# Kernel tuning notes

Measured on AMD Instinct MI355X. Metric: run time of the kernel, lower is better.

## Reference

```python
import jax, jax.numpy as jnp
import numpy as np

B, S, A, C = 32, 52, 3, 80  # batch, grid, anchors-per-cell, classes
EPS_LOG = 1e-16
EPS_IOU = 1e-6
L_CLASS, L_NOOBJ, L_OBJ, L_BOX = 1.0, 10.0, 1.0, 10.0


def setup_inputs() -> dict:
    key = jax.random.key(0)
    k_obj, k_xy, k_wh, k_cls, k_pred, k_anc = jax.random.split(key, 6)
    # target (B,S,S,3,6): [obj_flag, x, y, w, h, class_id]
    obj = (jax.random.uniform(k_obj, (B, S, S, A)) < 0.05).astype(jnp.float32)
    xy = jax.random.uniform(k_xy, (B, S, S, A, 2))
    wh = jax.random.uniform(k_wh, (B, S, S, A, 2), minval=0.1, maxval=2.0)
    cls = jax.random.randint(k_cls, (B, S, S, A), 0, C).astype(jnp.float32)
    target = jnp.concatenate([obj[..., None], xy, wh, cls[..., None]], axis=-1)
    pred = jax.random.normal(k_pred, (B, S, S, A * (C + 5)), dtype=jnp.float32)
    anchors = jax.random.uniform(k_anc, (A, 2), minval=0.5, maxval=2.0)
    return {"target": target, "pred": pred, "anchors": anchors}


def _iou_midpoint(b1, b2):
    # boxes [..., 4] = (cx, cy, w, h)
    b1x1, b1y1 = b1[..., 0] - b1[..., 2] / 2, b1[..., 1] - b1[..., 3] / 2
    b1x2, b1y2 = b1[..., 0] + b1[..., 2] / 2, b1[..., 1] + b1[..., 3] / 2
    b2x1, b2y1 = b2[..., 0] - b2[..., 2] / 2, b2[..., 1] - b2[..., 3] / 2
    b2x2, b2y2 = b2[..., 0] + b2[..., 2] / 2, b2[..., 1] + b2[..., 3] / 2
    iw = jnp.clip(jnp.minimum(b1x2, b2x2) - jnp.maximum(b1x1, b2x1), 0.0)
    ih = jnp.clip(jnp.minimum(b1y2, b2y2) - jnp.maximum(b1y1, b2y1), 0.0)
    inter = iw * ih
    a1 = jnp.abs((b1x2 - b1x1) * (b1y2 - b1y1))
    a2 = jnp.abs((b2x2 - b2x1) * (b2y2 - b2y1))
    return inter / (a1 + a2 - inter + EPS_IOU)


def reference(target, pred, anchors):
    b, s1, s2, k = pred.shape
    prediction = pred.reshape(b, s1, s2, A, k // A)  # (B,S,S,3,C+5)
    obj_f = (target[..., 0] == 1.0).astype(pred.dtype)     # (B,S,S,3)
    noobj_f = (target[..., 0] == 0.0).astype(pred.dtype)
    n_obj = jnp.maximum(jnp.sum(obj_f), 1.0)
    n_noobj = jnp.maximum(jnp.sum(noobj_f), 1.0)

    # ---- no-object BCE (from logits), mean over masked elems ----
    logit_o = prediction[..., 0]
    y = target[..., 0]
    bce = jnp.maximum(logit_o, 0.0) - logit_o * y + jnp.log1p(jnp.exp(-jnp.abs(logit_o)))
    noobjloss = jnp.sum(bce * noobj_f) / n_noobj

    # ---- class sparse CE (from logits), mean over obj cells ----
    logp = jax.nn.log_softmax(prediction[..., 5:], axis=-1)
    labels = target[..., 5].astype(jnp.int32)
    ce = -jnp.take_along_axis(logp, labels[..., None], axis=-1)[..., 0]
    classloss = jnp.sum(ce * obj_f) / n_obj

    # ---- box MSE in transformed space ----
    anc = anchors.reshape(1, 1, 1, A, 2)
    pred_xy = jax.nn.sigmoid(prediction[..., 1:3])
    tgt_wh_log = jnp.log(EPS_LOG + target[..., 3:5] / anc)
    tgt_box = jnp.concatenate([target[..., 1:3], tgt_wh_log], axis=-1)   # (B,S,S,3,4)
    pred_box_reg = jnp.concatenate([pred_xy, prediction[..., 3:5]], axis=-1)
    sq = (tgt_box - pred_box_reg) ** 2
    boxloss = jnp.sum(sq * obj_f[..., None]) / (4.0 * n_obj)

    # ---- objectness MSE against IoU (note: original code compares decoded
    # pred box to the LOG-transformed target wh, faithfully reproduced) ----
    box_pred = jnp.concatenate([pred_xy, jnp.exp(prediction[..., 3:5]) * anc], axis=-1)
    iou = _iou_midpoint(box_pred, tgt_box)                  # (B,S,S,3)
    objloss = jnp.sum(((iou * target[..., 0] - logit_o) ** 2) * obj_f) / n_obj

    return (L_NOOBJ * noobjloss + L_CLASS * classloss
            + L_BOX * boxloss + L_OBJ * objloss)
```

## Files before the change

### kernel.cpp

```cpp
#include <hip/hip_runtime.h>
#include <math.h>

#define BB 32
#define SS 52
#define AA 3
#define CC 80

constexpr int N_CELL = BB * SS * SS;
constexpr int N_ANCH = N_CELL * AA;
constexpr int BLOCK  = 256;
constexpr int NBLK   = N_ANCH / BLOCK;
constexpr int WSCOL  = 1024;

typedef float f4v __attribute__((ext_vector_type(4), aligned(4)));

__device__ __forceinline__ float fast_rcp(float x) {
    return __builtin_amdgcn_rcpf(x);
}


__global__ __launch_bounds__(BLOCK) void yolo_main(
    const float* __restrict__ target,
    const float* __restrict__ pred,
    const float* __restrict__ anchors,
    float* __restrict__ ws)
{
    const int tid  = threadIdx.x;
    const int n    = blockIdx.x * BLOCK + tid;
    const int lane = tid & 63;
    const int grp  = lane >> 4;
    const int l16  = lane & 15;

    const int cell = n / 3;
    const int a    = n - cell * 3;
    const int poff = cell * 255 + a * 85;

    __shared__ float ldsT[BLOCK * 6];
    __shared__ float ldsA[6];
    {
        const float4* tsrc = reinterpret_cast<const float4*>(target + (size_t)blockIdx.x * (BLOCK * 6));
        float4* tdst = reinterpret_cast<float4*>(ldsT);
        tdst[tid] = tsrc[tid];
        if (tid < 128) tdst[256 + tid] = tsrc[256 + tid];
        if (tid < 6)   ldsA[tid] = anchors[tid];
    }
    __syncthreads();

    const float* tr = ldsT + tid * 6;
    const float2 t01 = *reinterpret_cast<const float2*>(tr);
    const float2 t23 = *reinterpret_cast<const float2*>(tr + 2);
    const float2 t45 = *reinterpret_cast<const float2*>(tr + 4);
    const f4v   pq = *reinterpret_cast<const f4v*>(pred + poff);
    const float p4 = pred[poff + 4];
    const float p0 = pq.x, p1 = pq.y, p2 = pq.z, p3 = pq.w;
    const float aw = ldsA[a * 2 + 0];
    const float ah = ldsA[a * 2 + 1];

    const bool isobj   = (t01.x != 0.0f);
    const int  label_l = isobj ? (int)t45.y : 0;

    unsigned long long m = __ballot(isobj);
    unsigned long long m2 = m;
    int b0 = -1, b1 = -1, b2 = -1, b3 = -1;
    if (m2) { b0 = __ffsll(m2) - 1; m2 &= m2 - 1; }
    if (m2) { b1 = __ffsll(m2) - 1; m2 &= m2 - 1; }
    if (m2) { b2 = __ffsll(m2) - 1; m2 &= m2 - 1; }
    if (m2) { b3 = __ffsll(m2) - 1; m2 &= m2 - 1; }
    int  src0 = (grp == 0) ? b0 : (grp == 1) ? b1 : (grp == 2) ? b2 : b3;
    bool act0 = (src0 >= 0);
    int  s0   = act0 ? src0 : 0;
    int  offu0  = __shfl(poff, s0, 64) + 5;
    int  label0 = __shfl(label_l, s0, 64);
    const float* cl0 = pred + offu0;
    float w0 = 0.f, w1 = 0.f, w2 = 0.f, w3 = 0.f, w4 = 0.f;
    if (act0) {
        w0 = cl0[l16];      w1 = cl0[l16 + 16]; w2 = cl0[l16 + 32];
        w3 = cl0[l16 + 48]; w4 = cl0[l16 + 64];
    }

    float s_obj = 0.f, s_bce = 0.f, s_ce = 0.f, s_sq = 0.f, s_objt = 0.f;

    if (!isobj) {
        s_bce = fmaxf(p0, 0.0f) + __logf(1.0f + __expf(-fabsf(p0)));
    } else {
        s_obj = 1.0f;

        float px = fast_rcp(1.0f + __expf(-p1));
        float py = fast_rcp(1.0f + __expf(-p2));
        float tx = t01.y, ty = t23.x;
        float tw = __logf(1e-16f + t23.y * fast_rcp(aw));
        float th = __logf(1e-16f + t45.x * fast_rcp(ah));
        float dx = tx - px, dy = ty - py, dw = tw - p3, dh = th - p4;
        s_sq = dx * dx + dy * dy + dw * dw + dh * dh;

        float bw = __expf(p3) * aw;
        float bh = __expf(p4) * ah;
        float b1x1 = px - bw * 0.5f, b1x2 = px + bw * 0.5f;
        float b1y1 = py - bh * 0.5f, b1y2 = py + bh * 0.5f;
        float b2x1 = tx - tw * 0.5f, b2x2 = tx + tw * 0.5f;
        float b2y1 = ty - th * 0.5f, b2y2 = ty + th * 0.5f;
        float iw = fmaxf(fminf(b1x2, b2x2) - fmaxf(b1x1, b2x1), 0.0f);
        float ih = fmaxf(fminf(b1y2, b2y2) - fmaxf(b1y1, b2y1), 0.0f);
        float inter = iw * ih;
        float a1 = fabsf((b1x2 - b1x1) * (b1y2 - b1y1));
        float a2 = fabsf((b2x2 - b2x1) * (b2y2 - b2y1));
        float iou = inter * fast_rcp(a1 + a2 - inter + 1e-6f);
        float d = iou - p0;
        s_objt = d * d;
    }

    if (m) {
        float mx = fmaxf(fmaxf(fmaxf(w0, w1), fmaxf(w2, w3)), w4);
        #pragma unroll
        for (int o = 8; o > 0; o >>= 1) mx = fmaxf(mx, __shfl_xor(mx, o, 16));

        float se = __expf(w0 - mx) + __expf(w1 - mx) + __expf(w2 - mx)
                 + __expf(w3 - mx) + __expf(w4 - mx);
        #pragma unroll
        for (int o = 8; o > 0; o >>= 1) se += __shfl_xor(se, o, 16);

        int r  = label0 >> 4;
        float cand = (r == 0) ? w0 : (r == 1) ? w1 : (r == 2) ? w2
                   : (r == 3) ? w3 : w4;
        float cll  = __shfl(cand, (grp << 4) + (label0 & 15), 64);

        if (act0 && l16 == 0) s_ce += (mx + __logf(se)) - cll;
    }

    while (m2) {
        int c0 = -1, c1 = -1, c2 = -1, c3 = -1;
        if (m2) { c0 = __ffsll(m2) - 1; m2 &= m2 - 1; }
        if (m2) { c1 = __ffsll(m2) - 1; m2 &= m2 - 1; }
        if (m2) { c2 = __ffsll(m2) - 1; m2 &= m2 - 1; }
        if (m2) { c3 = __ffsll(m2) - 1; m2 &= m2 - 1; }
        int src = (grp == 0) ? c0 : (grp == 1) ? c1 : (grp == 2) ? c2 : c3;
        bool active = (src >= 0);
        int s = active ? src : 0;
        int offu  = __shfl(poff, s, 64) + 5;
        int label = __shfl(label_l, s, 64);
        const float* cl = pred + offu;

        float v0 = 0.f, v1 = 0.f, v2 = 0.f, v3 = 0.f, v4 = 0.f;
        if (active) {
            v0 = cl[l16];      v1 = cl[l16 + 16]; v2 = cl[l16 + 32];
            v3 = cl[l16 + 48]; v4 = cl[l16 + 64];
        }

        float mx = fmaxf(fmaxf(fmaxf(v0, v1), fmaxf(v2, v3)), v4);
        #pragma unroll
        for (int o = 8; o > 0; o >>= 1) mx = fmaxf(mx, __shfl_xor(mx, o, 16));

        float se = __expf(v0 - mx) + __expf(v1 - mx) + __expf(v2 - mx)
                 + __expf(v3 - mx) + __expf(v4 - mx);
        #pragma unroll
        for (int o = 8; o > 0; o >>= 1) se += __shfl_xor(se, o, 16);

        int r  = label >> 4;
        float cand = (r == 0) ? v0 : (r == 1) ? v1 : (r == 2) ? v2
                   : (r == 3) ? v3 : v4;
        float cll  = __shfl(cand, (grp << 4) + (label & 15), 64);

        if (active && l16 == 0) s_ce += (mx + __logf(se)) - cll;
    }

    #pragma unroll
    for (int off = 32; off > 0; off >>= 1) {
        s_obj  += __shfl_down(s_obj,  off, 64);
        s_bce  += __shfl_down(s_bce,  off, 64);
        s_sq   += __shfl_down(s_sq,   off, 64);
        s_objt += __shfl_down(s_objt, off, 64);
    }
    s_ce += __shfl_down(s_ce, 32, 64);
    s_ce += __shfl_down(s_ce, 16, 64);

    __shared__ float red[4][5];
    int wave = tid >> 6;
    if ((tid & 63) == 0) {
        red[wave][0] = s_obj; red[wave][1] = s_bce; red[wave][2] = s_ce;
        red[wave][3] = s_sq;  red[wave][4] = s_objt;
    }
    __syncthreads();
    if (tid < 5) {
        float v = red[0][tid] + red[1][tid] + red[2][tid] + red[3][tid];
        ws[tid * WSCOL + blockIdx.x] = v;
    }
}

__global__ __launch_bounds__(256) void yolo_final(const float* __restrict__ ws,
                                                  float* __restrict__ out) {
    float acc[5] = {0.f, 0.f, 0.f, 0.f, 0.f};
    #pragma unroll
    for (int r = 0; r < 4; ++r) {
        int b = threadIdx.x + r * 256;
        if (b < NBLK) {
            #pragma unroll
            for (int k = 0; k < 5; ++k) acc[k] += ws[k * WSCOL + b];
        }
    }
    #pragma unroll
    for (int off = 32; off > 0; off >>= 1) {
        #pragma unroll
        for (int k = 0; k < 5; ++k) acc[k] += __shfl_down(acc[k], off, 64);
    }
    __shared__ float red[4][5];
    int wave = threadIdx.x >> 6;
    if ((threadIdx.x & 63) == 0) {
        #pragma unroll
        for (int k = 0; k < 5; ++k) red[wave][k] = acc[k];
    }
    __syncthreads();
    if (threadIdx.x == 0) {
        float t[5];
        #pragma unroll
        for (int k = 0; k < 5; ++k)
            t[k] = red[0][k] + red[1][k] + red[2][k] + red[3][k];
        float n_obj   = fmaxf(t[0], 1.0f);
        float n_noobj = fmaxf((float)N_ANCH - t[0], 1.0f);
        float noobjloss = t[1] / n_noobj;
        float classloss = t[2] / n_obj;
        float boxloss   = t[3] / (4.0f * n_obj);
        float objloss   = t[4] / n_obj;
        out[0] = 10.0f * noobjloss + 1.0f * classloss + 10.0f * boxloss + 1.0f * objloss;
    }
}

extern "C" void kernel_launch(void* const* d_in, const int* in_sizes, int n_in,
                              void* d_out, int out_size, void* d_ws, size_t ws_size,
                              hipStream_t stream) {
    const float* target  = (const float*)d_in[0];
    const float* pred    = (const float*)d_in[1];
    const float* anchors = (const float*)d_in[2];
    float* out = (float*)d_out;
    float* ws  = (float*)d_ws;

    hipLaunchKernelGGL(yolo_main, dim3(NBLK), dim3(BLOCK), 0, stream,
                       target, pred, anchors, ws);

    hipLaunchKernelGGL(yolo_final, dim3(1), dim3(256), 0, stream, ws, out);
}
```

Before: 17.89 us.

## Fuse final reduction into main kernel via atomics and last-block completion counter

Drops the separate single-block finalize kernel. Each block atomically adds its five partial sums into one of 16 padded buckets and bumps a per-bucket arrival counter, and the last block to arrive reads the buckets and writes the loss. This removes a second kernel launch and its dependency gap, but adds a memset of the workspace, contention on the global atomics, and a reliance on the ordering given by s_waitcnt plus relaxed loads. Summing floats through atomics also makes the result order-dependent, so it is no longer deterministic.

```diff
diff --git a/kernel.cpp b/kernel.cpp
--- a/kernel.cpp
+++ b/kernel.cpp
@@ -10,7 +10,8 @@
 constexpr int N_ANCH = N_CELL * AA;
 constexpr int BLOCK  = 256;
 constexpr int NBLK   = N_ANCH / BLOCK;
-constexpr int WSCOL  = 1024;
+constexpr int NBUCK  = 16;
+
 
 typedef float f4v __attribute__((ext_vector_type(4), aligned(4)));
 
@@ -18,12 +19,12 @@
     return __builtin_amdgcn_rcpf(x);
 }
 
-
-__global__ __launch_bounds__(BLOCK) void yolo_main(
+__global__ __launch_bounds__(BLOCK) void yolo_fused(
     const float* __restrict__ target,
     const float* __restrict__ pred,
     const float* __restrict__ anchors,
-    float* __restrict__ ws)
+    float* __restrict__ ws,
+    float* __restrict__ out)
 {
     const int tid  = threadIdx.x;
     const int n    = blockIdx.x * BLOCK + tid;
@@ -37,12 +38,14 @@
 
     __shared__ float ldsT[BLOCK * 6];
     __shared__ float ldsA[6];
+    __shared__ int   s_fin;
     {
         const float4* tsrc = reinterpret_cast<const float4*>(target + (size_t)blockIdx.x * (BLOCK * 6));
         float4* tdst = reinterpret_cast<float4*>(ldsT);
         tdst[tid] = tsrc[tid];
         if (tid < 128) tdst[256 + tid] = tsrc[256 + tid];
         if (tid < 6)   ldsA[tid] = anchors[tid];
+        if (tid == 0)  s_fin = 0;
     }
     __syncthreads();
 
@@ -180,47 +183,49 @@
         red[wave][3] = s_sq;  red[wave][4] = s_objt;
     }
     __syncthreads();
+
+    const int bkt = blockIdx.x & (NBUCK - 1);
     if (tid < 5) {
         float v = red[0][tid] + red[1][tid] + red[2][tid] + red[3][tid];
-        ws[tid * WSCOL + blockIdx.x] = v;
-    }
-}
-
-__global__ __launch_bounds__(256) void yolo_final(const float* __restrict__ ws,
-                                                  float* __restrict__ out) {
-    float acc[5] = {0.f, 0.f, 0.f, 0.f, 0.f};
-    #pragma unroll
-    for (int r = 0; r < 4; ++r) {
-        int b = threadIdx.x + r * 256;
-        if (b < NBLK) {
+        atomicAdd(ws + (bkt * 5 + tid) * 32, v);
+    }
+    asm volatile("s_waitcnt vmcnt(0)" ::: "memory");
+
+    if (tid == 0) {
+        unsigned int quota = (bkt < 6) ? 64u : 63u;
+        unsigned int* sub    = reinterpret_cast<unsigned int*>(ws + 2560 + bkt * 32);
+        unsigned int* master = reinterpret_cast<unsigned int*>(ws + 3072);
+        unsigned int old = atomicAdd(sub, 1u);
+        if (old == quota - 1u) {
+            unsigned int old2 = atomicAdd(master, 1u);
+            if (old2 == (unsigned int)(NBUCK - 1)) s_fin = 1;
+        }
+    }
+    __syncthreads();
+
+    if (s_fin) {
+        __shared__ float vals[80];
+        if (tid < 80) {
+            vals[tid] = __hip_atomic_load(ws + tid * 32, __ATOMIC_RELAXED,
+                                          __HIP_MEMORY_SCOPE_AGENT);
+        }
+        __syncthreads();
+        if (tid == 0) {
+            float t[5] = {0.f, 0.f, 0.f, 0.f, 0.f};
             #pragma unroll
-            for (int k = 0; k < 5; ++k) acc[k] += ws[k * WSCOL + b];
-        }
-    }
-    #pragma unroll
-    for (int off = 32; off > 0; off >>= 1) {
-        #pragma unroll
-        for (int k = 0; k < 5; ++k) acc[k] += __shfl_down(acc[k], off, 64);
-    }
-    __shared__ float red[4][5];
-    int wave = threadIdx.x >> 6;
-    if ((threadIdx.x & 63) == 0) {
-        #pragma unroll
-        for (int k = 0; k < 5; ++k) red[wave][k] = acc[k];
-    }
-    __syncthreads();
-    if (threadIdx.x == 0) {
-        float t[5];
-        #pragma unroll
-        for (int k = 0; k < 5; ++k)
-            t[k] = red[0][k] + red[1][k] + red[2][k] + red[3][k];
-        float n_obj   = fmaxf(t[0], 1.0f);
-        float n_noobj = fmaxf((float)N_ANCH - t[0], 1.0f);
-        float noobjloss = t[1] / n_noobj;
-        float classloss = t[2] / n_obj;
-        float boxloss   = t[3] / (4.0f * n_obj);
-        float objloss   = t[4] / n_obj;
-        out[0] = 10.0f * noobjloss + 1.0f * classloss + 10.0f * boxloss + 1.0f * objloss;
+            for (int b = 0; b < NBUCK; ++b) {
+                #pragma unroll
+                for (int k = 0; k < 5; ++k) t[k] += vals[b * 5 + k];
+            }
+            float n_obj   = fmaxf(t[0], 1.0f);
+            float n_noobj = fmaxf((float)N_ANCH - t[0], 1.0f);
+            float noobjloss = t[1] / n_noobj;
+            float classloss = t[2] / n_obj;
+            float boxloss   = t[3] / (4.0f * n_obj);
+            float objloss   = t[4] / n_obj;
+            out[0] = 10.0f * noobjloss + 1.0f * classloss
+                   + 10.0f * boxloss + 1.0f * objloss;
+        }
     }
 }
 
@@ -233,8 +238,8 @@
     float* out = (float*)d_out;
     float* ws  = (float*)d_ws;
 
-    hipLaunchKernelGGL(yolo_main, dim3(NBLK), dim3(BLOCK), 0, stream,
-                       target, pred, anchors, ws);
-
-    hipLaunchKernelGGL(yolo_final, dim3(1), dim3(256), 0, stream, ws, out);
+    hipMemsetAsync(ws, 0, 12544, stream);
+
+    hipLaunchKernelGGL(yolo_fused, dim3(NBLK), dim3(BLOCK), 0, stream,
+                       target, pred, anchors, ws, out);
 }
```

After: 22.06 us. +23.3%, slower.
